# Kernel tuning notes

Hardware: AMD Instinct MI355X
Metric: run time of the kernel (lower is better)

Reference implementation:

```python
import jax, jax.numpy as jnp
import numpy as np

N = 50000
E = 800000
C_IN, C_HID, C_OUT = 128, 64, 1


def setup_inputs() -> dict:
    key = jax.random.key(0)
    ks = jax.random.split(key, 8)
    x = jax.random.normal(ks[0], (N, C_IN), dtype=jnp.float32)
    edge_index = jax.random.randint(ks[1], (2, E), 0, N, dtype=jnp.int64)
    # GCNConv linear params (glorot-ish scaling)
    W1 = jax.random.normal(ks[2], (C_IN, C_HID), dtype=jnp.float32) / np.sqrt(C_IN)
    b1 = jnp.zeros((C_HID,), dtype=jnp.float32)
    W2 = jax.random.normal(ks[3], (C_HID, C_HID), dtype=jnp.float32) / np.sqrt(C_HID)
    b2 = jnp.zeros((C_HID,), dtype=jnp.float32)
    W3 = jax.random.normal(ks[4], (C_HID, C_OUT), dtype=jnp.float32) / np.sqrt(C_HID)
    b3 = jnp.zeros((C_OUT,), dtype=jnp.float32)
    return {"x": x, "edge_index": edge_index, "W1": W1, "b1": b1,
            "W2": W2, "b2": b2, "W3": W3, "b3": b3}


def _gcn_norm(edge_index, num_nodes):
    # Add self-loops, compute symmetric normalization D^{-1/2} A D^{-1/2}
    loop = jnp.arange(num_nodes, dtype=edge_index.dtype)
    src = jnp.concatenate([edge_index[0], loop])  # message sources
    dst = jnp.concatenate([edge_index[1], loop])  # message targets
    ones = jnp.ones(src.shape[0], dtype=jnp.float32)
    deg = jax.ops.segment_sum(ones, dst, num_segments=num_nodes)
    dis = jnp.where(deg > 0, jax.lax.rsqrt(jnp.maximum(deg, 1.0)), 0.0)
    norm = dis[src] * dis[dst]  # [E+N]
    return src, dst, norm


def _gcn_conv(h, src, dst, norm, W, b, num_nodes):
    h = h @ W                                  # [N, C_out]
    msg = h[src] * norm[:, None]               # gather + scale, [E+N, C_out]
    out = jax.ops.segment_sum(msg, dst, num_segments=num_nodes)  # scatter-add
    return out + b


def reference(x, edge_index, W1, b1, W2, b2, W3, b3):
    num_nodes = x.shape[0]
    src, dst, norm = _gcn_norm(edge_index, num_nodes)
    leaky = lambda v: jnp.where(v >= 0, v, 0.01 * v)
    h = _gcn_conv(x, src, dst, norm, W1, b1, num_nodes)
    h = leaky(h)
    h = _gcn_conv(h, src, dst, norm, W2, b2, num_nodes)
    h = leaky(h)
    h = _gcn_conv(h, src, dst, norm, W3, b3, num_nodes)
    return h
```

## Files before the change

### kernel.cpp

```cpp
#include <hip/hip_runtime.h>

#define CIN 128
#define CHID 64
#define CSTRIDE 64

__device__ __forceinline__ float leaky(float v) { return v >= 0.f ? v : 0.01f * v; }
__device__ __forceinline__ float bcast(float v, int k) {
    return __int_as_float(__builtin_amdgcn_readlane(__float_as_int(v), k));
}
__device__ __forceinline__ void acc4(float4& a, const float4 v) {
    a.x += v.x; a.y += v.y; a.z += v.z; a.w += v.w;
}
__device__ __forceinline__ void xorred(float4& a) {
    a.x += __shfl_xor(a.x, 16, 64); a.y += __shfl_xor(a.y, 16, 64);
    a.z += __shfl_xor(a.z, 16, 64); a.w += __shfl_xor(a.w, 16, 64);
    a.x += __shfl_xor(a.x, 32, 64); a.y += __shfl_xor(a.y, 32, 64);
    a.z += __shfl_xor(a.z, 32, 64); a.w += __shfl_xor(a.w, 32, 64);
}

__global__ void k_deg(const int* __restrict__ dst, const int* __restrict__ src,
                      int* __restrict__ deg, unsigned short* __restrict__ csr,
                      int E, int nps, int N) {
    const int shard = blockIdx.x & 7;
    const int chunk = blockIdx.x >> 3;
    const int nchunks = gridDim.x >> 3;
    const int lo = shard * nps;
    const int hi = min(lo + nps, N);
    const int estride = nchunks * 256;
    for (int e = chunk * 256 + threadIdx.x; e < E; e += estride) {
        int d = dst[e];
        if (d >= lo && d < hi) {
            int slot = atomicAdd(&deg[d], 1);
            if (slot < CSTRIDE) csr[(d << 6) + slot] = (unsigned short)src[e];
        }
    }
}

__global__ __launch_bounds__(256) void k_gemm1(
    const float* __restrict__ x, const float* __restrict__ W,
    const int* __restrict__ deg, float* __restrict__ hp, int N) {
    const int wave = threadIdx.x >> 6, lane = threadIdx.x & 63;
    float w[CIN];
#pragma unroll
    for (int k = 0; k < CIN; ++k) w[k] = W[k * CHID + lane];
    const int stride = gridDim.x * 4;
    for (int n = blockIdx.x * 4 + wave; n < N; n += stride) {
        float x0 = x[(size_t)n * CIN + lane];
        float x1 = x[(size_t)n * CIN + 64 + lane];
        float acc0 = 0.f, acc1 = 0.f;
#pragma unroll
        for (int k = 0; k < 64; k += 2) {
            acc0 = fmaf(bcast(x0, k),     w[k],     acc0);
            acc1 = fmaf(bcast(x0, k + 1), w[k + 1], acc1);
        }
#pragma unroll
        for (int k = 0; k < 64; k += 2) {
            acc0 = fmaf(bcast(x1, k),     w[64 + k],     acc0);
            acc1 = fmaf(bcast(x1, k + 1), w[64 + k + 1], acc1);
        }
        float dn = rsqrtf((float)(deg[n] + 1));
        hp[(size_t)n * CHID + lane] = dn * (acc0 + acc1);
    }
}

__global__ __launch_bounds__(256) void kG1(
    const unsigned short* __restrict__ csr, const int* __restrict__ deg,
    const float* __restrict__ hp, const float* __restrict__ W2,
    const float* __restrict__ b1, float* __restrict__ hp2, int N) {
    const int wave = threadIdx.x >> 6, lane = threadIdx.x & 63;
    const int g = lane >> 4, sl = lane & 15;
    float w[CHID];
#pragma unroll
    for (int k = 0; k < CHID; ++k) w[k] = W2[k * CHID + lane];
    const float4 bb = ((const float4*)b1)[sl];
    const float4* __restrict__ hpq = (const float4*)hp;
    const int stride = gridDim.x * 4;
    const int n0 = blockIdx.x * 4 + wave;
    int d = 0, c0 = 0, c1 = 0, c2 = 0, c3 = 0;
    if (n0 < N) {
        d = deg[n0];
        int base = n0 << 6;
        c0 = csr[base + g];      c1 = csr[base + g + 4];
        c2 = csr[base + g + 8];  c3 = csr[base + g + 12];
    }
    for (int n = n0; n < N; n += stride) {
        const int n2 = n + stride;
        int dN = 0, e0 = 0, e1 = 0, e2 = 0, e3 = 0;
        if (n2 < N) {
            dN = deg[n2];
            int b2 = n2 << 6;
            e0 = csr[b2 + g];      e1 = csr[b2 + g + 4];
            e2 = csr[b2 + g + 8];  e3 = csr[b2 + g + 12];
        }
        const int dc = d, base = n << 6;
        float4 a0 = make_float4(0.f, 0.f, 0.f, 0.f), a1 = a0, a2 = a0, a3 = a0;
        if (g == 0) a0 = hpq[(size_t)n * 16 + sl];
        if (g < dc)      acc4(a0, hpq[(size_t)c0 * 16 + sl]);
        if (g + 4 < dc)  acc4(a1, hpq[(size_t)c1 * 16 + sl]);
        if (g + 8 < dc)  acc4(a2, hpq[(size_t)c2 * 16 + sl]);
        if (g + 12 < dc) acc4(a3, hpq[(size_t)c3 * 16 + sl]);
        for (int b = g + 16; b < dc; b += 16) {
            { int s = csr[base + b];      acc4(a0, hpq[(size_t)s * 16 + sl]); }
            if (b + 4 < dc)  { int s = csr[base + b + 4];  acc4(a1, hpq[(size_t)s * 16 + sl]); }
            if (b + 8 < dc)  { int s = csr[base + b + 8];  acc4(a2, hpq[(size_t)s * 16 + sl]); }
            if (b + 12 < dc) { int s = csr[base + b + 12]; acc4(a3, hpq[(size_t)s * 16 + sl]); }
        }
        acc4(a0, a1); acc4(a2, a3); acc4(a0, a2);
        xorred(a0);
        float dn = rsqrtf((float)(dc + 1));
        float4 gv;
        gv.x = leaky(dn * a0.x + bb.x);
        gv.y = leaky(dn * a0.y + bb.y);
        gv.z = leaky(dn * a0.z + bb.z);
        gv.w = leaky(dn * a0.w + bb.w);
        float acc0 = 0.f, acc1 = 0.f;
#pragma unroll
        for (int i = 0; i < 16; ++i) {
            acc0 = fmaf(bcast(gv.x, i), w[4 * i + 0], acc0);
            acc1 = fmaf(bcast(gv.y, i), w[4 * i + 1], acc1);
            acc0 = fmaf(bcast(gv.z, i), w[4 * i + 2], acc0);
            acc1 = fmaf(bcast(gv.w, i), w[4 * i + 3], acc1);
        }
        hp2[(size_t)n * CHID + lane] = dn * (acc0 + acc1);
        d = dN; c0 = e0; c1 = e1; c2 = e2; c3 = e3;
    }
}

__global__ __launch_bounds__(256) void kG2(
    const unsigned short* __restrict__ csr, const int* __restrict__ deg,
    const float* __restrict__ hp, const float* __restrict__ b2,
    const float* __restrict__ W3, float* __restrict__ hp3, int N) {
    const int wave = threadIdx.x >> 6, lane = threadIdx.x & 63;
    const int g = lane >> 4, sl = lane & 15;
    const float4 bb = ((const float4*)b2)[sl];
    const float4 w3 = ((const float4*)W3)[sl];
    const float4* __restrict__ hpq = (const float4*)hp;
    const int stride = gridDim.x * 4;
    const int n0 = blockIdx.x * 4 + wave;
    int d = 0, c0 = 0, c1 = 0, c2 = 0, c3 = 0;
    if (n0 < N) {
        d = deg[n0];
        int base = n0 << 6;
        c0 = csr[base + g];      c1 = csr[base + g + 4];
        c2 = csr[base + g + 8];  c3 = csr[base + g + 12];
    }
    for (int n = n0; n < N; n += stride) {
        const int n2 = n + stride;
        int dN = 0, e0 = 0, e1 = 0, e2 = 0, e3 = 0;
        if (n2 < N) {
            dN = deg[n2];
            int b2i = n2 << 6;
            e0 = csr[b2i + g];      e1 = csr[b2i + g + 4];
            e2 = csr[b2i + g + 8];  e3 = csr[b2i + g + 12];
        }
        const int dc = d, base = n << 6;
        float4 a0 = make_float4(0.f, 0.f, 0.f, 0.f), a1 = a0, a2 = a0, a3 = a0;
        if (g == 0) a0 = hpq[(size_t)n * 16 + sl];
        if (g < dc)      acc4(a0, hpq[(size_t)c0 * 16 + sl]);
        if (g + 4 < dc)  acc4(a1, hpq[(size_t)c1 * 16 + sl]);
        if (g + 8 < dc)  acc4(a2, hpq[(size_t)c2 * 16 + sl]);
        if (g + 12 < dc) acc4(a3, hpq[(size_t)c3 * 16 + sl]);
        for (int b = g + 16; b < dc; b += 16) {
            { int s = csr[base + b];      acc4(a0, hpq[(size_t)s * 16 + sl]); }
            if (b + 4 < dc)  { int s = csr[base + b + 4];  acc4(a1, hpq[(size_t)s * 16 + sl]); }
            if (b + 8 < dc)  { int s = csr[base + b + 8];  acc4(a2, hpq[(size_t)s * 16 + sl]); }
            if (b + 12 < dc) { int s = csr[base + b + 12]; acc4(a3, hpq[(size_t)s * 16 + sl]); }
        }
        acc4(a0, a1); acc4(a2, a3); acc4(a0, a2);
        xorred(a0);
        float dn = rsqrtf((float)(dc + 1));
        float t = leaky(dn * a0.x + bb.x) * w3.x
                + leaky(dn * a0.y + bb.y) * w3.y
                + leaky(dn * a0.z + bb.z) * w3.z
                + leaky(dn * a0.w + bb.w) * w3.w;
        t += __shfl_xor(t, 1, 64); t += __shfl_xor(t, 2, 64);
        t += __shfl_xor(t, 4, 64); t += __shfl_xor(t, 8, 64);
        if (lane == 0) hp3[n] = dn * t;
        d = dN; c0 = e0; c1 = e1; c2 = e2; c3 = e3;
    }
}

__global__ void kG3(const unsigned short* __restrict__ csr, const int* __restrict__ deg,
                    const float* __restrict__ hp3, const float* __restrict__ b3,
                    float* __restrict__ out, int N) {
    int t = blockIdx.x * 256 + threadIdx.x;
    int node = t >> 4, sl = t & 15;
    if (node >= N) return;
    int d = deg[node], base = node << 6;
    float acc = (sl == 0) ? hp3[node] : 0.f;
    for (int i = sl; i < d; i += 16) acc += hp3[(int)csr[base + i]];
#pragma unroll
    for (int off = 8; off > 0; off >>= 1) acc += __shfl_down(acc, off, 16);
    if (sl == 0) out[node] = rsqrtf((float)(d + 1)) * acc + b3[0];
}

extern "C" void kernel_launch(void* const* d_in, const int* in_sizes, int n_in,
                              void* d_out, int out_size, void* d_ws, size_t ws_size,
                              hipStream_t stream) {
    const float* x  = (const float*)d_in[0];
    const int*   ei = (const int*)d_in[1];
    const float* W1 = (const float*)d_in[2];
    const float* b1 = (const float*)d_in[3];
    const float* W2 = (const float*)d_in[4];
    const float* b2 = (const float*)d_in[5];
    const float* W3 = (const float*)d_in[6];
    const float* b3 = (const float*)d_in[7];

    const int N = in_sizes[0] / CIN;
    const int E = in_sizes[1] / 2;
    const int* src = ei;
    const int* dst = ei + E;
    const int nps = (N + 7) / 8;

    char* w = (char*)d_ws;
    auto take = [&](size_t bytes) { char* p = w; w += (bytes + 255) & ~(size_t)255; return p; };
    int*            deg = (int*)take((size_t)N * 4);
    unsigned short* csr = (unsigned short*)take((size_t)N * CSTRIDE * 2);
    float*          A   = (float*)take((size_t)N * CHID * 4);
    float*          B   = (float*)take((size_t)N * CHID * 4);
    float*          hp3 = (float*)take((size_t)N * 4);

    hipMemsetAsync(deg, 0, (size_t)N * 4, stream);

    k_deg  <<<2048, 256, 0, stream>>>(dst, src, deg, csr, E, nps, N);
    k_gemm1<<<1024, 256, 0, stream>>>(x, W1, deg, A, N);
    kG1    <<<2048, 256, 0, stream>>>(csr, deg, A, W2, b1, B, N);
    kG2    <<<2048, 256, 0, stream>>>(csr, deg, B, b2, W3, hp3, N);
    kG3    <<<(N * 16 + 255) / 256, 256, 0, stream>>>(csr, deg, hp3, b3, (float*)d_out, N);
}
```

Before: 224.4 us.

## Deepen software pipeline in GCN gather kernels to prefetch neighbor features

kG1 and kG2 now use a two-stage prefetch. While node n is processed, the first four neighbor feature rows and the self row of the next node are already loaded into registers, and the CSR indices and degree of the node after that are being fetched. Invalid slots are pointed at the node itself so the loads stay unconditional. The goal is to hide the latency of the dependent index-then-gather chain. In exchange, the extra float4 registers (about 20 more VGPRs) may lower occupancy, especially in kG1, which already holds 64 weight registers.

```diff
diff --git a/kernel.cpp b/kernel.cpp
--- a/kernel.cpp
+++ b/kernel.cpp
@@ -76,29 +76,57 @@
     const float4* __restrict__ hpq = (const float4*)hp;
     const int stride = gridDim.x * 4;
     const int n0 = blockIdx.x * 4 + wave;
-    int d = 0, c0 = 0, c1 = 0, c2 = 0, c3 = 0;
+    const float4 z = make_float4(0.f, 0.f, 0.f, 0.f);
+
+    int dA = 0;
+    float4 vsA = z, vA0 = z, vA1 = z, vA2 = z, vA3 = z;
+    int dB = 0, cB0 = 0, cB1 = 0, cB2 = 0, cB3 = 0;
+
     if (n0 < N) {
-        d = deg[n0];
+        dA = deg[n0];
         int base = n0 << 6;
-        c0 = csr[base + g];      c1 = csr[base + g + 4];
-        c2 = csr[base + g + 8];  c3 = csr[base + g + 12];
-    }
+        int t0 = csr[base + g], t1 = csr[base + g + 4];
+        int t2 = csr[base + g + 8], t3 = csr[base + g + 12];
+        int s0 = (g < dA) ? t0 : n0,      s1 = (g + 4 < dA) ? t1 : n0;
+        int s2 = (g + 8 < dA) ? t2 : n0,  s3 = (g + 12 < dA) ? t3 : n0;
+        vsA = hpq[(size_t)n0 * 16 + sl];
+        vA0 = hpq[(size_t)s0 * 16 + sl]; vA1 = hpq[(size_t)s1 * 16 + sl];
+        vA2 = hpq[(size_t)s2 * 16 + sl]; vA3 = hpq[(size_t)s3 * 16 + sl];
+    }
+    {
+        const int n1 = n0 + stride;
+        if (n1 < N) {
+            dB = deg[n1];
+            int base = n1 << 6;
+            cB0 = csr[base + g];      cB1 = csr[base + g + 4];
+            cB2 = csr[base + g + 8];  cB3 = csr[base + g + 12];
+        }
+    }
+
     for (int n = n0; n < N; n += stride) {
-        const int n2 = n + stride;
-        int dN = 0, e0 = 0, e1 = 0, e2 = 0, e3 = 0;
+        const int nn = n + stride, n2 = nn + stride;
+        float4 vsB = z, vB0 = z, vB1 = z, vB2 = z, vB3 = z;
+        if (nn < N) {
+            int s0 = (g < dB) ? cB0 : nn,      s1 = (g + 4 < dB) ? cB1 : nn;
+            int s2 = (g + 8 < dB) ? cB2 : nn,  s3 = (g + 12 < dB) ? cB3 : nn;
+            vsB = hpq[(size_t)nn * 16 + sl];
+            vB0 = hpq[(size_t)s0 * 16 + sl]; vB1 = hpq[(size_t)s1 * 16 + sl];
+            vB2 = hpq[(size_t)s2 * 16 + sl]; vB3 = hpq[(size_t)s3 * 16 + sl];
+        }
+        int dC = 0, cC0 = 0, cC1 = 0, cC2 = 0, cC3 = 0;
         if (n2 < N) {
-            dN = deg[n2];
-            int b2 = n2 << 6;
-            e0 = csr[b2 + g];      e1 = csr[b2 + g + 4];
-            e2 = csr[b2 + g + 8];  e3 = csr[b2 + g + 12];
-        }
-        const int dc = d, base = n << 6;
-        float4 a0 = make_float4(0.f, 0.f, 0.f, 0.f), a1 = a0, a2 = a0, a3 = a0;
-        if (g == 0) a0 = hpq[(size_t)n * 16 + sl];
-        if (g < dc)      acc4(a0, hpq[(size_t)c0 * 16 + sl]);
-        if (g + 4 < dc)  acc4(a1, hpq[(size_t)c1 * 16 + sl]);
-        if (g + 8 < dc)  acc4(a2, hpq[(size_t)c2 * 16 + sl]);
-        if (g + 12 < dc) acc4(a3, hpq[(size_t)c3 * 16 + sl]);
+            dC = deg[n2];
+            int base2 = n2 << 6;
+            cC0 = csr[base2 + g];      cC1 = csr[base2 + g + 4];
+            cC2 = csr[base2 + g + 8];  cC3 = csr[base2 + g + 12];
+        }
+        const int dc = dA, base = n << 6;
+        float4 a0 = z, a1 = z, a2 = z, a3 = z;
+        if (g == 0)      a0 = vsA;
+        if (g < dc)      acc4(a0, vA0);
+        if (g + 4 < dc)  acc4(a1, vA1);
+        if (g + 8 < dc)  acc4(a2, vA2);
+        if (g + 12 < dc) acc4(a3, vA3);
         for (int b = g + 16; b < dc; b += 16) {
             { int s = csr[base + b];      acc4(a0, hpq[(size_t)s * 16 + sl]); }
             if (b + 4 < dc)  { int s = csr[base + b + 4];  acc4(a1, hpq[(size_t)s * 16 + sl]); }
@@ -122,7 +150,8 @@
             acc1 = fmaf(bcast(gv.w, i), w[4 * i + 3], acc1);
         }
         hp2[(size_t)n * CHID + lane] = dn * (acc0 + acc1);
-        d = dN; c0 = e0; c1 = e1; c2 = e2; c3 = e3;
+        dA = dB; vsA = vsB; vA0 = vB0; vA1 = vB1; vA2 = vB2; vA3 = vB3;
+        dB = dC; cB0 = cC0; cB1 = cC1; cB2 = cC2; cB3 = cC3;
     }
 }
 
@@ -137,29 +166,57 @@
     const float4* __restrict__ hpq = (const float4*)hp;
     const int stride = gridDim.x * 4;
     const int n0 = blockIdx.x * 4 + wave;
-    int d = 0, c0 = 0, c1 = 0, c2 = 0, c3 = 0;
+    const float4 z = make_float4(0.f, 0.f, 0.f, 0.f);
+
+    int dA = 0;
+    float4 vsA = z, vA0 = z, vA1 = z, vA2 = z, vA3 = z;
+    int dB = 0, cB0 = 0, cB1 = 0, cB2 = 0, cB3 = 0;
+
     if (n0 < N) {
-        d = deg[n0];
+        dA = deg[n0];
         int base = n0 << 6;
-        c0 = csr[base + g];      c1 = csr[base + g + 4];
-        c2 = csr[base + g + 8];  c3 = csr[base + g + 12];
-    }
+        int t0 = csr[base + g], t1 = csr[base + g + 4];
+        int t2 = csr[base + g + 8], t3 = csr[base + g + 12];
+        int s0 = (g < dA) ? t0 : n0,      s1 = (g + 4 < dA) ? t1 : n0;
+        int s2 = (g + 8 < dA) ? t2 : n0,  s3 = (g + 12 < dA) ? t3 : n0;
+        vsA = hpq[(size_t)n0 * 16 + sl];
+        vA0 = hpq[(size_t)s0 * 16 + sl]; vA1 = hpq[(size_t)s1 * 16 + sl];
+        vA2 = hpq[(size_t)s2 * 16 + sl]; vA3 = hpq[(size_t)s3 * 16 + sl];
+    }
+    {
+        const int n1 = n0 + stride;
+        if (n1 < N) {
+            dB = deg[n1];
+            int base = n1 << 6;
+            cB0 = csr[base + g];      cB1 = csr[base + g + 4];
+            cB2 = csr[base + g + 8];  cB3 = csr[base + g + 12];
+        }
+    }
+
     for (int n = n0; n < N; n += stride) {
-        const int n2 = n + stride;
-        int dN = 0, e0 = 0, e1 = 0, e2 = 0, e3 = 0;
+        const int nn = n + stride, n2 = nn + stride;
+        float4 vsB = z, vB0 = z, vB1 = z, vB2 = z, vB3 = z;
+        if (nn < N) {
+            int s0 = (g < dB) ? cB0 : nn,      s1 = (g + 4 < dB) ? cB1 : nn;
+            int s2 = (g + 8 < dB) ? cB2 : nn,  s3 = (g + 12 < dB) ? cB3 : nn;
+            vsB = hpq[(size_t)nn * 16 + sl];
+            vB0 = hpq[(size_t)s0 * 16 + sl]; vB1 = hpq[(size_t)s1 * 16 + sl];
+            vB2 = hpq[(size_t)s2 * 16 + sl]; vB3 = hpq[(size_t)s3 * 16 + sl];
+        }
+        int dC = 0, cC0 = 0, cC1 = 0, cC2 = 0, cC3 = 0;
         if (n2 < N) {
-            dN = deg[n2];
-            int b2i = n2 << 6;
-            e0 = csr[b2i + g];      e1 = csr[b2i + g + 4];
-            e2 = csr[b2i + g + 8];  e3 = csr[b2i + g + 12];
-        }
-        const int dc = d, base = n << 6;
-        float4 a0 = make_float4(0.f, 0.f, 0.f, 0.f), a1 = a0, a2 = a0, a3 = a0;
-        if (g == 0) a0 = hpq[(size_t)n * 16 + sl];
-        if (g < dc)      acc4(a0, hpq[(size_t)c0 * 16 + sl]);
-        if (g + 4 < dc)  acc4(a1, hpq[(size_t)c1 * 16 + sl]);
-        if (g + 8 < dc)  acc4(a2, hpq[(size_t)c2 * 16 + sl]);
-        if (g + 12 < dc) acc4(a3, hpq[(size_t)c3 * 16 + sl]);
+            dC = deg[n2];
+            int base2 = n2 << 6;
+            cC0 = csr[base2 + g];      cC1 = csr[base2 + g + 4];
+            cC2 = csr[base2 + g + 8];  cC3 = csr[base2 + g + 12];
+        }
+        const int dc = dA, base = n << 6;
+        float4 a0 = z, a1 = z, a2 = z, a3 = z;
+        if (g == 0)      a0 = vsA;
+        if (g < dc)      acc4(a0, vA0);
+        if (g + 4 < dc)  acc4(a1, vA1);
+        if (g + 8 < dc)  acc4(a2, vA2);
+        if (g + 12 < dc) acc4(a3, vA3);
         for (int b = g + 16; b < dc; b += 16) {
             { int s = csr[base + b];      acc4(a0, hpq[(size_t)s * 16 + sl]); }
             if (b + 4 < dc)  { int s = csr[base + b + 4];  acc4(a1, hpq[(size_t)s * 16 + sl]); }
@@ -176,7 +233,8 @@
         t += __shfl_xor(t, 1, 64); t += __shfl_xor(t, 2, 64);
         t += __shfl_xor(t, 4, 64); t += __shfl_xor(t, 8, 64);
         if (lane == 0) hp3[n] = dn * t;
-        d = dN; c0 = e0; c1 = e1; c2 = e2; c3 = e3;
+        dA = dB; vsA = vsB; vA0 = vB0; vA1 = vB1; vA2 = vB2; vA3 = vB3;
+        dB = dC; cB0 = cC0; cB1 = cC1; cB2 = cC2; cB3 = cC3;
     }
 }
 
```

Result: no change. 225.9 us (+0.6%).
